# Kernel optimization log

Measured on AMD Instinct MI355X. Metric: run time of the kernel, lower is better.

The kernel has to match this reference:

```python
import jax, jax.numpy as jnp
import numpy as np

N = 4096  # square [B, T+1] as required by original indexing (T = shape[0], indexed on dim 1)
GAMMA = 0.99

def setup_inputs() -> dict:
    key = jax.random.key(0)
    ks = jax.random.split(key, 6)
    shape = (N, N)
    names = ["Q", "expected_target_Q", "target_Q", "rewards",
             "target_policy_probs", "behaviour_policy_probs"]
    return {n: jax.random.normal(k, shape, dtype=jnp.float32) for n, k in zip(names, ks)}

def _retrace_loss(Q, expected_target_Q, target_Q, rewards,
                  target_policy_probs, behaviour_policy_probs):
    rewards = rewards * 100.0
    # retrace weights c_t = exp(min(log pi - log b, 0)) = min(1, pi/b)
    c_ret = jnp.exp(jnp.minimum(target_policy_probs - behaviour_policy_probs, 0.0))
    T = Q.shape[0]  # faithful to original (square inputs => equals time length)
    last = target_Q[:, T - 1]  # Q_ret[:, -1] = target_Q[:, -1]
    # reverse-time linear recurrence via a single scan:
    # Q_ret[t-1] = r[t-1] + gamma*c[t]*(Q_ret[t] - target_Q[t]) + gamma*E[t]
    xs = (rewards[:, :T - 1].T[::-1],          # [T-1, B], t-1 = T-2 .. 0
          c_ret[:, 1:T].T[::-1],               # c[t],  t = T-1 .. 1
          target_Q[:, 1:T].T[::-1],
          expected_target_Q[:, 1:T].T[::-1])

    def step(q_next, x):
        r, c, tq, eq = x
        q = r + GAMMA * c * (q_next - tq) + GAMMA * eq
        return q, q

    _, qs = jax.lax.scan(step, last, xs)       # qs: [T-1, B] for t = T-2 .. 0
    Q_ret = jnp.concatenate([qs[::-1].T, last[:, None]], axis=1)  # [B, T]
    Q_ret = jax.lax.stop_gradient(Q_ret)       # computed under torch.no_grad()
    return jnp.mean((Q - Q_ret) ** 2)

def reference(Q, expected_target_Q, target_Q, rewards,
              target_policy_probs, behaviour_policy_probs):
    return _retrace_loss(Q, expected_target_Q, target_Q, rewards,
                         target_policy_probs, behaviour_policy_probs)
```

## Files before the change

kernel.cpp:

```cpp
#include <hip/hip_runtime.h>


#define NROWS 4096
#define TLEN  4096
#define BLOCK 256
#define EPT   16

__global__ __launch_bounds__(BLOCK) void retrace_main(
    const float* __restrict__ Q,
    const float* __restrict__ eQ,
    const float* __restrict__ tQ,
    const float* __restrict__ rw,
    const float* __restrict__ tpp,
    const float* __restrict__ bpp,
    double* __restrict__ partials)
{
    constexpr float G = 0.99f;
    __shared__ float sWA[4], sWB[4];
    __shared__ float sRed[4];

    const int tid  = threadIdx.x;
    const int lane = tid & 63;
    const int wv   = tid >> 6;
    const long long base = (long long)blockIdx.x * TLEN;
    const int ua = (TLEN - EPT) - EPT * tid;

    float4 Rv4[4], Tv4[4], Pv4[4], Qt4[4], Ev4[4], Qm4[4];
    #pragma unroll
    for (int g = 0; g < 4; ++g) Rv4[g] = *(const float4*)(rw  + base + ua + 4 * g);
    #pragma unroll
    for (int g = 0; g < 4; ++g) Tv4[g] = *(const float4*)(tpp + base + ua + 4 * g);
    #pragma unroll
    for (int g = 0; g < 4; ++g) Pv4[g] = *(const float4*)(bpp + base + ua + 4 * g);
    #pragma unroll
    for (int g = 0; g < 4; ++g) Qt4[g] = *(const float4*)(tQ  + base + ua + 4 * g);
    #pragma unroll
    for (int g = 0; g < 4; ++g) Ev4[g] = *(const float4*)(eQ  + base + ua + 4 * g);
    #pragma unroll
    for (int g = 0; g < 4; ++g) Qm4[g] = *(const float4*)(Q   + base + ua + 4 * g);

    const bool bnd = (lane == 0) && (tid != 0);
    float bt = 0.f, bp = 0.f, bq = 0.f, be = 0.f;
    if (bnd) {
        bt = tpp[base + ua + 16];
        bp = bpp[base + ua + 16];
        bq = tQ [base + ua + 16];
        be = eQ [base + ua + 16];
    }

    float rv[16], tv[16], pv[16], qv[16], ev[16], qm[16];
    #pragma unroll
    for (int g = 0; g < 4; ++g) {
        rv[4*g+0]=Rv4[g].x; rv[4*g+1]=Rv4[g].y; rv[4*g+2]=Rv4[g].z; rv[4*g+3]=Rv4[g].w;
        tv[4*g+0]=Tv4[g].x; tv[4*g+1]=Tv4[g].y; tv[4*g+2]=Tv4[g].z; tv[4*g+3]=Tv4[g].w;
        pv[4*g+0]=Pv4[g].x; pv[4*g+1]=Pv4[g].y; pv[4*g+2]=Pv4[g].z; pv[4*g+3]=Pv4[g].w;
        qv[4*g+0]=Qt4[g].x; qv[4*g+1]=Qt4[g].y; qv[4*g+2]=Qt4[g].z; qv[4*g+3]=Qt4[g].w;
        ev[4*g+0]=Ev4[g].x; ev[4*g+1]=Ev4[g].y; ev[4*g+2]=Ev4[g].z; ev[4*g+3]=Ev4[g].w;
        qm[4*g+0]=Qm4[g].x; qm[4*g+1]=Qm4[g].y; qm[4*g+2]=Qm4[g].z; qm[4*g+3]=Qm4[g].w;
    }

    float Aa[16], Bb[16];
    #pragma unroll
    for (int m = 1; m <= 15; ++m) {
        const float c  = __expf(fminf(tv[m] - pv[m], 0.0f));
        const float gc = G * c;
        const float f  = fmaf(-gc, qv[m], G * ev[m]);
        Aa[m-1] = gc;
        Bb[m-1] = fmaf(100.0f, rv[m-1], f);
    }
    {
        float t16 = __shfl_up(tv[0], 1, 64);
        float p16 = __shfl_up(pv[0], 1, 64);
        float q16 = __shfl_up(qv[0], 1, 64);
        float e16 = __shfl_up(ev[0], 1, 64);
        if (bnd) { t16 = bt; p16 = bp; q16 = bq; e16 = be; }
        if (tid == 0) {
            Aa[15] = 0.0f;
            Bb[15] = qv[15];
        } else {
            const float c  = __expf(fminf(t16 - p16, 0.0f));
            const float gc = G * c;
            const float f  = fmaf(-gc, q16, G * e16);
            Aa[15] = gc;
            Bb[15] = fmaf(100.0f, rv[15], f);
        }
    }

    float Ac = 1.0f, Bc = 0.0f;
    #pragma unroll
    for (int k = 0; k < EPT; ++k) {
        const int idx = 15 - k;
        Bc = fmaf(Aa[idx], Bc, Bb[idx]);
        Ac = Aa[idx] * Ac;
    }

    float Ai = Ac, Bi = Bc;
    #pragma unroll
    for (int off = 1; off < 64; off <<= 1) {
        const float Ap = __shfl_up(Ai, off, 64);
        const float Bp = __shfl_up(Bi, off, 64);
        if (lane >= off) {
            Bi = fmaf(Ai, Bp, Bi);
            Ai = Ai * Ap;
        }
    }

    if (lane == 63) { sWA[wv] = Ai; sWB[wv] = Bi; }
    __syncthreads();
    float Bp = 0.0f;
    #pragma unroll
    for (int j = 0; j < 3; ++j)
        if (j < wv) Bp = fmaf(sWA[j], Bp, sWB[j]);

    float Ae = __shfl_up(Ai, 1, 64);
    float Be = __shfl_up(Bi, 1, 64);
    if (lane == 0) { Ae = 1.0f; Be = 0.0f; }
    float y = fmaf(Ae, Bp, Be);

    float acc = 0.0f;
    #pragma unroll
    for (int k = 0; k < EPT; ++k) {
        const int idx = 15 - k;
        y = fmaf(Aa[idx], y, Bb[idx]);
        const float d = qm[idx] - y;
        acc = fmaf(d, d, acc);
    }

    #pragma unroll
    for (int off = 32; off > 0; off >>= 1)
        acc += __shfl_down(acc, off, 64);
    if (lane == 0) sRed[wv] = acc;
    __syncthreads();
    if (tid == 0) {
        const float s = sRed[0] + sRed[1] + sRed[2] + sRed[3];
        partials[blockIdx.x] = (double)s;
    }
}

__global__ __launch_bounds__(BLOCK) void retrace_finalize(
    const double* __restrict__ partials, float* __restrict__ out)
{
    __shared__ double sRed[BLOCK / 64];
    double s = 0.0;
    for (int i = threadIdx.x; i < NROWS; i += BLOCK) s += partials[i];
    #pragma unroll
    for (int off = 32; off > 0; off >>= 1)
        s += __shfl_down(s, off, 64);
    if ((threadIdx.x & 63) == 0) sRed[threadIdx.x >> 6] = s;
    __syncthreads();
    if (threadIdx.x == 0) {
        const double tot = sRed[0] + sRed[1] + sRed[2] + sRed[3];
        out[0] = (float)(tot / ((double)NROWS * (double)TLEN));
    }
}

extern "C" void kernel_launch(void* const* d_in, const int* in_sizes, int n_in,
                              void* d_out, int out_size, void* d_ws, size_t ws_size,
                              hipStream_t stream)
{
    const float* Q   = (const float*)d_in[0];
    const float* eQ  = (const float*)d_in[1];
    const float* tQ  = (const float*)d_in[2];
    const float* rw  = (const float*)d_in[3];
    const float* tpp = (const float*)d_in[4];
    const float* bpp = (const float*)d_in[5];
    double* partials = (double*)d_ws;

    retrace_main<<<NROWS, BLOCK, 0, stream>>>(Q, eQ, tQ, rw, tpp, bpp, partials);
    retrace_finalize<<<1, BLOCK, 0, stream>>>(partials, (float*)d_out);
}
```

Before: 339.7 us.

## Use 1024-thread blocks with four elements per thread for the row scan

```diff
diff --git a/kernel.cpp b/kernel.cpp
--- a/kernel.cpp
+++ b/kernel.cpp
@@ -3,8 +3,9 @@
 
 #define NROWS 4096
 #define TLEN  4096
-#define BLOCK 256
-#define EPT   16
+#define BLOCK 1024
+#define EPT   4
+#define NWAVES (BLOCK / 64)
 
 __global__ __launch_bounds__(BLOCK) void retrace_main(
     const float* __restrict__ Q,
@@ -16,8 +17,9 @@
     double* __restrict__ partials)
 {
     constexpr float G = 0.99f;
-    __shared__ float sWA[4], sWB[4];
-    __shared__ float sRed[4];
+    __shared__ float sT[NWAVES], sP[NWAVES], sQ[NWAVES], sE[NWAVES];
+    __shared__ float sWA[NWAVES], sWB[NWAVES];
+    __shared__ float sRed[NWAVES];
 
     const int tid  = threadIdx.x;
     const int lane = tid & 63;
@@ -25,71 +27,53 @@
     const long long base = (long long)blockIdx.x * TLEN;
     const int ua = (TLEN - EPT) - EPT * tid;
 
-    float4 Rv4[4], Tv4[4], Pv4[4], Qt4[4], Ev4[4], Qm4[4];
-    #pragma unroll
-    for (int g = 0; g < 4; ++g) Rv4[g] = *(const float4*)(rw  + base + ua + 4 * g);
-    #pragma unroll
-    for (int g = 0; g < 4; ++g) Tv4[g] = *(const float4*)(tpp + base + ua + 4 * g);
-    #pragma unroll
-    for (int g = 0; g < 4; ++g) Pv4[g] = *(const float4*)(bpp + base + ua + 4 * g);
-    #pragma unroll
-    for (int g = 0; g < 4; ++g) Qt4[g] = *(const float4*)(tQ  + base + ua + 4 * g);
-    #pragma unroll
-    for (int g = 0; g < 4; ++g) Ev4[g] = *(const float4*)(eQ  + base + ua + 4 * g);
-    #pragma unroll
-    for (int g = 0; g < 4; ++g) Qm4[g] = *(const float4*)(Q   + base + ua + 4 * g);
+    const float4 R4  = *(const float4*)(rw  + base + ua);
+    const float4 T4  = *(const float4*)(tpp + base + ua);
+    const float4 P4  = *(const float4*)(bpp + base + ua);
+    const float4 Tq4 = *(const float4*)(tQ  + base + ua);
+    const float4 E4  = *(const float4*)(eQ  + base + ua);
+    const float4 Qm4 = *(const float4*)(Q   + base + ua);
 
-    const bool bnd = (lane == 0) && (tid != 0);
-    float bt = 0.f, bp = 0.f, bq = 0.f, be = 0.f;
-    if (bnd) {
-        bt = tpp[base + ua + 16];
-        bp = bpp[base + ua + 16];
-        bq = tQ [base + ua + 16];
-        be = eQ [base + ua + 16];
+    if (lane == 63) { sT[wv] = T4.x; sP[wv] = P4.x; sQ[wv] = Tq4.x; sE[wv] = E4.x; }
+    __syncthreads();
+
+    float t4v = __shfl_up(T4.x,  1, 64);
+    float p4v = __shfl_up(P4.x,  1, 64);
+    float q4v = __shfl_up(Tq4.x, 1, 64);
+    float e4v = __shfl_up(E4.x,  1, 64);
+    if (lane == 0 && wv > 0) {
+        t4v = sT[wv - 1]; p4v = sP[wv - 1]; q4v = sQ[wv - 1]; e4v = sE[wv - 1];
     }
 
-    float rv[16], tv[16], pv[16], qv[16], ev[16], qm[16];
+    const float rv[4] = {R4.x,  R4.y,  R4.z,  R4.w};
+    const float tv[4] = {T4.x,  T4.y,  T4.z,  T4.w};
+    const float pv[4] = {P4.x,  P4.y,  P4.z,  P4.w};
+    const float qv[4] = {Tq4.x, Tq4.y, Tq4.z, Tq4.w};
+    const float ev[4] = {E4.x,  E4.y,  E4.z,  E4.w};
+    const float qm[4] = {Qm4.x, Qm4.y, Qm4.z, Qm4.w};
+
+    float Aa[EPT], Bb[EPT];
     #pragma unroll
-    for (int g = 0; g < 4; ++g) {
-        rv[4*g+0]=Rv4[g].x; rv[4*g+1]=Rv4[g].y; rv[4*g+2]=Rv4[g].z; rv[4*g+3]=Rv4[g].w;
-        tv[4*g+0]=Tv4[g].x; tv[4*g+1]=Tv4[g].y; tv[4*g+2]=Tv4[g].z; tv[4*g+3]=Tv4[g].w;
-        pv[4*g+0]=Pv4[g].x; pv[4*g+1]=Pv4[g].y; pv[4*g+2]=Pv4[g].z; pv[4*g+3]=Pv4[g].w;
-        qv[4*g+0]=Qt4[g].x; qv[4*g+1]=Qt4[g].y; qv[4*g+2]=Qt4[g].z; qv[4*g+3]=Qt4[g].w;
-        ev[4*g+0]=Ev4[g].x; ev[4*g+1]=Ev4[g].y; ev[4*g+2]=Ev4[g].z; ev[4*g+3]=Ev4[g].w;
-        qm[4*g+0]=Qm4[g].x; qm[4*g+1]=Qm4[g].y; qm[4*g+2]=Qm4[g].z; qm[4*g+3]=Qm4[g].w;
-    }
-
-    float Aa[16], Bb[16];
-    #pragma unroll
-    for (int m = 1; m <= 15; ++m) {
+    for (int m = 1; m <= EPT - 1; ++m) {
         const float c  = __expf(fminf(tv[m] - pv[m], 0.0f));
         const float gc = G * c;
-        const float f  = fmaf(-gc, qv[m], G * ev[m]);
-        Aa[m-1] = gc;
-        Bb[m-1] = fmaf(100.0f, rv[m-1], f);
+        Aa[m - 1] = gc;
+        Bb[m - 1] = fmaf(100.0f, rv[m - 1], fmaf(-gc, qv[m], G * ev[m]));
     }
-    {
-        float t16 = __shfl_up(tv[0], 1, 64);
-        float p16 = __shfl_up(pv[0], 1, 64);
-        float q16 = __shfl_up(qv[0], 1, 64);
-        float e16 = __shfl_up(ev[0], 1, 64);
-        if (bnd) { t16 = bt; p16 = bp; q16 = bq; e16 = be; }
-        if (tid == 0) {
-            Aa[15] = 0.0f;
-            Bb[15] = qv[15];
-        } else {
-            const float c  = __expf(fminf(t16 - p16, 0.0f));
-            const float gc = G * c;
-            const float f  = fmaf(-gc, q16, G * e16);
-            Aa[15] = gc;
-            Bb[15] = fmaf(100.0f, rv[15], f);
-        }
+    if (tid == 0) {
+        Aa[EPT - 1] = 0.0f;
+        Bb[EPT - 1] = qv[EPT - 1];
+    } else {
+        const float c  = __expf(fminf(t4v - p4v, 0.0f));
+        const float gc = G * c;
+        Aa[EPT - 1] = gc;
+        Bb[EPT - 1] = fmaf(100.0f, rv[EPT - 1], fmaf(-gc, q4v, G * e4v));
     }
 
     float Ac = 1.0f, Bc = 0.0f;
     #pragma unroll
     for (int k = 0; k < EPT; ++k) {
-        const int idx = 15 - k;
+        const int idx = EPT - 1 - k;
         Bc = fmaf(Aa[idx], Bc, Bb[idx]);
         Ac = Aa[idx] * Ac;
     }
@@ -109,7 +93,7 @@
     __syncthreads();
     float Bp = 0.0f;
     #pragma unroll
-    for (int j = 0; j < 3; ++j)
+    for (int j = 0; j < NWAVES - 1; ++j)
         if (j < wv) Bp = fmaf(sWA[j], Bp, sWB[j]);
 
     float Ae = __shfl_up(Ai, 1, 64);
@@ -120,7 +104,7 @@
     float acc = 0.0f;
     #pragma unroll
     for (int k = 0; k < EPT; ++k) {
-        const int idx = 15 - k;
+        const int idx = EPT - 1 - k;
         y = fmaf(Aa[idx], y, Bb[idx]);
         const float d = qm[idx] - y;
         acc = fmaf(d, d, acc);
@@ -132,17 +116,19 @@
     if (lane == 0) sRed[wv] = acc;
     __syncthreads();
     if (tid == 0) {
-        const float s = sRed[0] + sRed[1] + sRed[2] + sRed[3];
+        float s = 0.0f;
+        #pragma unroll
+        for (int j = 0; j < NWAVES; ++j) s += sRed[j];
         partials[blockIdx.x] = (double)s;
     }
 }
 
-__global__ __launch_bounds__(BLOCK) void retrace_finalize(
+__global__ __launch_bounds__(256) void retrace_finalize(
     const double* __restrict__ partials, float* __restrict__ out)
 {
-    __shared__ double sRed[BLOCK / 64];
+    __shared__ double sRed[4];
     double s = 0.0;
-    for (int i = threadIdx.x; i < NROWS; i += BLOCK) s += partials[i];
+    for (int i = threadIdx.x; i < NROWS; i += 256) s += partials[i];
     #pragma unroll
     for (int off = 32; off > 0; off >>= 1)
         s += __shfl_down(s, off, 64);
@@ -167,5 +153,5 @@
     double* partials = (double*)d_ws;
 
     retrace_main<<<NROWS, BLOCK, 0, stream>>>(Q, eQ, tQ, rw, tpp, bpp, partials);
-    retrace_finalize<<<1, BLOCK, 0, stream>>>(partials, (float*)d_out);
+    retrace_finalize<<<1, 256, 0, stream>>>(partials, (float*)d_out);
 }
```

After: 341.7 us. No clear change (+0.6%).
